# Performance work log

Measured on AMD Instinct MI355X. Metric: run time of the kernel, lower is better.

Reference implementation:

```python
import jax, jax.numpy as jnp
import numpy as np

N = 200000          # number of nodes (objects)
H = 64              # hidden_size
ARITIES = [1, 2, 3] # arity per relation
NTUP = [250000, 250000, 250000]  # ground atoms per relation


def setup_inputs() -> dict:
    key = jax.random.key(0)
    ks = jax.random.split(key, 32)
    inp = {"node_states": jax.random.normal(ks[0], (N, H), jnp.float32)}
    i = 1
    for r, (a, t) in enumerate(zip(ARITIES, NTUP)):
        inp[f"rel{r}_idx"] = jax.random.randint(ks[i], (t * a,), 0, N, dtype=jnp.int32).astype(jnp.int64); i += 1
        d = a * H
        s = (2.0 / d) ** 0.5
        inp[f"w1_r{r}"] = jax.random.normal(ks[i], (d, d), jnp.float32) * s; i += 1
        inp[f"b1_r{r}"] = jnp.zeros((d,), jnp.float32)
        inp[f"w2_r{r}"] = jax.random.normal(ks[i], (d, d), jnp.float32) * s; i += 1
        inp[f"b2_r{r}"] = jnp.zeros((d,), jnp.float32)
    su = (1.0 / (2 * H)) ** 0.5
    inp["wu1"] = jax.random.normal(ks[i], (2 * H, 2 * H), jnp.float32) * su; i += 1
    inp["bu1"] = jnp.zeros((2 * H,), jnp.float32)
    inp["wu2"] = jax.random.normal(ks[i], (2 * H, H), jnp.float32) * su
    inp["bu2"] = jnp.zeros((H,), jnp.float32)
    return inp


def reference(node_states, rel0_idx, rel1_idx, rel2_idx,
              w1_r0, b1_r0, w2_r0, b2_r0,
              w1_r1, b1_r1, w2_r1, b2_r1,
              w1_r2, b1_r2, w2_r2, b2_r2,
              wu1, bu1, wu2, bu2):
    sum_msg = jnp.zeros_like(node_states)
    rels = [(ARITIES[0], rel0_idx, w1_r0, b1_r0, w2_r0, b2_r0),
            (ARITIES[1], rel1_idx, w1_r1, b1_r1, w2_r1, b2_r1),
            (ARITIES[2], rel2_idx, w1_r2, b1_r2, w2_r2, b2_r2)]
    for a, idx, w1, b1, w2, b2 in rels:
        # gather node states for each ground atom: [T, a*H]
        x = node_states[idx].reshape(-1, a * H)
        h = jax.nn.relu(x @ w1 + b1)
        msg = (h @ w2 + b2).reshape(-1, H)  # [T*a, H]
        # scatter-add messages back to their nodes
        sum_msg = sum_msg.at[idx].add(msg)
    z = jnp.concatenate([sum_msg, node_states], axis=1)  # [N, 2H]
    return jax.nn.relu(z @ wu1 + bu1) @ wu2 + bu2
```

## Files before the change

### kernel.cpp

```cpp
#include <hip/hip_runtime.h>

#define H 64

typedef __attribute__((ext_vector_type(8))) __bf16 bf16x8;
typedef __attribute__((ext_vector_type(4))) float f32x4;
typedef unsigned short u16;
typedef unsigned int u32;

union F8 { bf16x8 b; u16 u[8]; uint4 q; };

__device__ __forceinline__ u16 f2bf(float f) {
    union { __bf16 h; u16 u; } v; v.h = (__bf16)f; return v.u;
}
__device__ __forceinline__ float bf2f(u16 x) {
    return __uint_as_float((u32)x << 16);
}
__device__ __forceinline__ unsigned swz(int col, int k, int K) {
    return ((unsigned)(col * K + k) * 2u) ^ (((unsigned)col & 7u) << 4);
}

struct Seg { const float* src; unsigned dstBytes; int K; int N; };
struct Segs { Seg s[8]; };

__global__ __launch_bounds__(256) void conv_weights(Segs segs, char* out) {
    Seg sg = segs.s[blockIdx.y];
    int total = sg.K * sg.N;
    char* dst = out + sg.dstBytes;
    for (int e = blockIdx.x * 256 + threadIdx.x; e < total; e += gridDim.x * 256) {
        int k = e / sg.N, n = e % sg.N;
        *(u16*)(dst + swz(n, k, sg.K)) = f2bf(sg.src[e]);
    }
}

__global__ __launch_bounds__(256) void conv_nodes(const float4* __restrict__ src,
                                                  ushort4* __restrict__ dst, int n4) {
    for (int i = blockIdx.x * 256 + threadIdx.x; i < n4; i += gridDim.x * 256) {
        float4 f = src[i];
        ushort4 o;
        o.x = f2bf(f.x); o.y = f2bf(f.y); o.z = f2bf(f.z); o.w = f2bf(f.w);
        dst[i] = o;
    }
}

__global__ __launch_bounds__(512) void scan_blocks(u32* __restrict__ data,
                                                   u32* __restrict__ sums, int n) {
    __shared__ u32 s[512];
    int tid = threadIdx.x, i = blockIdx.x * 512 + tid;
    u32 v = (i < n) ? data[i] : 0u;
    s[tid] = v; __syncthreads();
    for (int d = 1; d < 512; d <<= 1) {
        u32 t = (tid >= d) ? s[tid - d] : 0u; __syncthreads();
        s[tid] += t; __syncthreads();
    }
    if (i < n) data[i] = s[tid] - v;
    if (tid == 511) sums[blockIdx.x] = s[511];
}

__global__ __launch_bounds__(512) void scan_sums(u32* __restrict__ sums, int nb) {
    __shared__ u32 s[512];
    int tid = threadIdx.x;
    u32 v = (tid < nb) ? sums[tid] : 0u;
    s[tid] = v; __syncthreads();
    for (int d = 1; d < 512; d <<= 1) {
        u32 t = (tid >= d) ? s[tid - d] : 0u; __syncthreads();
        s[tid] += t; __syncthreads();
    }
    if (tid < nb) sums[tid] = s[tid] - v;
}

__global__ __launch_bounds__(512) void scan_add(u32* __restrict__ data,
                                                const u32* __restrict__ sums, int n) {
    int i = blockIdx.x * 512 + threadIdx.x;
    if (i < n) data[i] += sums[blockIdx.x];
}

struct OFix {
    const int* idx0; const int* idx1; const int* idx2;
    int m0, m1, m2;
    const u32* base; const u32* pre; u32* ord;
};

__global__ __launch_bounds__(256) void ord_fix(OFix a) {
    const int Mtot = a.m0 + a.m1 + a.m2;
    for (int e = blockIdx.x * 256 + threadIdx.x; e < Mtot; e += gridDim.x * 256) {
        int lm = e, node;
        if (lm < a.m0) node = a.idx0[lm];
        else { lm -= a.m0; if (lm < a.m1) node = a.idx1[lm]; else node = a.idx2[lm - a.m1]; }
        a.ord[a.base[node] + a.pre[e]] = (u32)e;
    }
}

template<int A>
__device__ __forceinline__ void msg_body(
    const u16* __restrict__ nsb, const int* __restrict__ idx,
    const u16* __restrict__ w1T, const float* __restrict__ b1,
    const u16* __restrict__ w2T, const float* __restrict__ b2,
    u16* __restrict__ msgR, int T, int bid, u16* Wl, u16* h1)
{
    constexpr int D    = A * 64;
    constexpr int KS   = D / 32;
    constexpr int NT   = D / 16;
    constexpr bool DUAL = (A == 1);
    constexpr bool CS   = (A > 1);
    constexpr int RF   = CS ? 2 : 1;
    constexpr int WH   = (A == 3) ? 3 : 1;
    constexpr int NTH  = NT / WH;
    constexpr int NTW  = CS ? NTH / 2 : NTH;
    constexpr int COLH = D / WH;
    constexpr int NPF  = (DUAL ? 2 * D * D : COLH * D) / 8 / 512;
    constexpr int NB   = WH * NTW;

    const int tid  = threadIdx.x;
    const int lane = tid & 63;
    const int w    = tid >> 6;
    const int g    = lane >> 4;
    const int lr   = lane & 15;
    const int rg   = CS ? (w >> 1) : w;
    const int cg   = CS ? (w & 1) : 0;

    const int tile = bid * 128;

    auto stage = [&](const u16* gsrc) {
#pragma unroll
        for (int i = 0; i < NPF; ++i) {
            const u16* gp = gsrc + ((i * 512 + tid) << 3);
            u16* lp = Wl + ((i * 512 + (w << 6)) << 3);
            __builtin_amdgcn_global_load_lds(
                (const __attribute__((address_space(1))) void*)gp,
                (__attribute__((address_space(3))) void*)lp, 16, 0, 0);
        }
    };

    bf16x8 a1[RF][KS];
#pragma unroll
    for (int rf = 0; rf < RF; ++rf) {
        const int trow = tile + rg * (16 * RF) + rf * 16 + lr;
        const int tl   = trow < T ? trow : T - 1;
        int nodes[A];
#pragma unroll
        for (int s = 0; s < A; ++s) nodes[s] = idx[(long)tl * A + s];
#pragma unroll
        for (int kk = 0; kk < KS; ++kk) {
            const u16* p = nsb + (long)nodes[kk >> 1] * H + ((kk & 1) * 32 + g * 8);
            F8 t; t.q = *(const uint4*)p;
            a1[rf][kk] = t.b;
        }
    }

    float bias1[NB], bias2[NB];
#pragma unroll
    for (int i = 0; i < NB; ++i) {
        const int jg = (i / NTW) * NTH + cg * NTW + (i % NTW);
        bias1[i] = b1[jg * 16 + lr];
        bias2[i] = b2[jg * 16 + lr];
    }

#pragma unroll
    for (int hh = 0; hh < WH; ++hh) {
        stage(DUAL ? w1T : (w1T + (size_t)hh * COLH * D));
        asm volatile("s_waitcnt vmcnt(0)" ::: "memory");
        __syncthreads();

#pragma unroll
        for (int jl = 0; jl < NTW; ++jl) {
            const int jc = cg * NTW + jl;
            const int jg = hh * NTH + jc;
            f32x4 acc0 = {0.f, 0.f, 0.f, 0.f};
            f32x4 acc1 = {0.f, 0.f, 0.f, 0.f};
#pragma unroll
            for (int kk = 0; kk < KS; ++kk) {
                F8 bf; bf.q = *(const uint4*)((const char*)Wl + swz(jc * 16 + lr, kk * 32 + g * 8, D));
                acc0 = __builtin_amdgcn_mfma_f32_16x16x32_bf16(a1[0][kk], bf.b, acc0, 0, 0, 0);
                if constexpr (CS)
                    acc1 = __builtin_amdgcn_mfma_f32_16x16x32_bf16(a1[1][kk], bf.b, acc1, 0, 0, 0);
            }
#pragma unroll
            for (int r = 0; r < 4; ++r) {
                const int row0 = rg * (16 * RF) + g * 4 + r;
                float v0 = acc0[r] + bias1[hh * NTW + jl]; v0 = v0 > 0.f ? v0 : 0.f;
                *(u16*)((char*)h1 + swz(row0, jg * 16 + lr, D)) = f2bf(v0);
                if constexpr (CS) {
                    float v1 = acc1[r] + bias1[hh * NTW + jl]; v1 = v1 > 0.f ? v1 : 0.f;
                    *(u16*)((char*)h1 + swz(row0 + 16, jg * 16 + lr, D)) = f2bf(v1);
                }
            }
        }
        if constexpr (!DUAL) __syncthreads();
    }

    bf16x8 a2[RF][KS];
#pragma unroll
    for (int rf = 0; rf < RF; ++rf) {
        const int row = rg * (16 * RF) + rf * 16 + lr;
#pragma unroll
        for (int kk = 0; kk < KS; ++kk) {
            F8 t; t.q = *(const uint4*)((const char*)h1 + swz(row, kk * 32 + g * 8, D));
            a2[rf][kk] = t.b;
        }
    }

#pragma unroll
    for (int hh = 0; hh < WH; ++hh) {
        if constexpr (!DUAL) {
            stage(w2T + (size_t)hh * COLH * D);
            asm volatile("s_waitcnt vmcnt(0)" ::: "memory");
            __syncthreads();
        }
        const char* W2base = DUAL ? (const char*)(Wl + D * D) : (const char*)Wl;

#pragma unroll
        for (int jl = 0; jl < NTW; ++jl) {
            const int jc = cg * NTW + jl;
            const int jg = hh * NTH + jc;
            f32x4 acc0 = {0.f, 0.f, 0.f, 0.f};
            f32x4 acc1 = {0.f, 0.f, 0.f, 0.f};
#pragma unroll
            for (int kk = 0; kk < KS; ++kk) {
                F8 bf; bf.q = *(const uint4*)(W2base + swz(jc * 16 + lr, kk * 32 + g * 8, D));
                acc0 = __builtin_amdgcn_mfma_f32_16x16x32_bf16(a2[0][kk], bf.b, acc0, 0, 0, 0);
                if constexpr (CS)
                    acc1 = __builtin_amdgcn_mfma_f32_16x16x32_bf16(a2[1][kk], bf.b, acc1, 0, 0, 0);
            }
            const int gc   = jg * 16 + lr;
            const int slot = gc >> 6;
            const int cs_  = gc & 63;
#pragma unroll
            for (int r = 0; r < 4; ++r) {
                const int a0 = rg * (16 * RF) + g * 4 + r;
                const int m0 = a0 * A + slot;
                unsigned b0 = (((unsigned)(m0 * 64 + cs_)) * 2u) ^ (((unsigned)m0 & 7u) << 4);
                *(u16*)((char*)h1 + b0) = f2bf(acc0[r] + bias2[hh * NTW + jl]);
                if constexpr (CS) {
                    const int m1 = (a0 + 16) * A + slot;
                    unsigned b1x = (((unsigned)(m1 * 64 + cs_)) * 2u) ^ (((unsigned)m1 & 7u) << 4);
                    *(u16*)((char*)h1 + b1x) = f2bf(acc1[r] + bias2[hh * NTW + jl]);
                }
            }
        }
        if constexpr (!DUAL) { if (hh + 1 < WH) __syncthreads(); }
    }

    if constexpr (CS) {
        __syncthreads();
        const int mbase = tile * A;
        constexpr int CH = 128 * A * 16;
#pragma unroll
        for (int i = 0; i < CH / 512; ++i) {
            const int c    = i * 512 + tid;
            const int row  = c >> 4;
            const int atom = row / A;
            if (tile + atom < T) {
                unsigned byte = (((unsigned)(row * 64 + (c & 15) * 4)) * 2u) ^ (((unsigned)row & 7u) << 4);
                uint2 v = *(const uint2*)((const char*)h1 + byte);
                *(uint2*)(msgR + (size_t)(mbase + row) * 64 + (c & 15) * 4) = v;
            }
        }
    } else {
        const int  mbase = (tile + w * 16) * A;
        const bool full  = (tile + 128 <= T);
#pragma unroll
        for (int i = 0; i < 16 * A; i += 4) {
            int ml   = i + (lane >> 4);
            int mrow = w * 16 * A + ml;
            bool ok  = full || ((tile + w * 16 + ml / A) < T);
            if (ok) {
                unsigned byte = (((unsigned)(mrow * 64 + (lane & 15) * 4)) * 2u) ^ (((unsigned)mrow & 7u) << 4);
                uint2 v = *(const uint2*)((const char*)h1 + byte);
                *(uint2*)(msgR + (size_t)((tile * A) + mrow) * 64 + (lane & 15) * 4) = v;
            }
        }
    }
}

struct MegaA {
    const u16* nsb;
    const int* idx0; const int* idx1; const int* idx2;
    int m0, m1, m2, t0, t1, t2;
    u32* cnt; u32* pre;
    const u16 *w10, *w20, *w11, *w21, *w12, *w22;
    const float *b10, *b20, *b11, *b21, *b12, *b22;
    u16* msgu;
    int nrank, nb2, nb1, nb0, striped;
};

__global__ __launch_bounds__(512, 4) void mega_kernel(MegaA a) {
    __shared__ __align__(16) u16 sm[36864];
    const int bx = blockIdx.x;
    int kind, id;
    if (a.striped) {
        const int strip = 4 * a.nrank;
        if (bx < strip) {
            if ((bx & 3) == 3) { kind = 1; id = bx >> 2; }
            else               { kind = 0; id = bx - (bx >> 2); }
        } else { kind = 0; id = bx - a.nrank; }
    } else {
        if (bx < a.nrank) { kind = 1; id = bx; }
        else              { kind = 0; id = bx - a.nrank; }
    }

    if (kind == 1) {
        const int Mtot = a.m0 + a.m1 + a.m2;
        for (int e = id * 512 + (int)threadIdx.x; e < Mtot; e += a.nrank * 512) {
            int lm = e, node;
            if (lm < a.m0) node = a.idx0[lm];
            else { lm -= a.m0; if (lm < a.m1) node = a.idx1[lm]; else node = a.idx2[lm - a.m1]; }
            a.pre[e] = atomicAdd(a.cnt + node, 1u);
        }
        return;
    }

    const int nmsg = a.nb2 + a.nb1 + a.nb0;
    if (id >= nmsg) return;
    if (id < a.nb2)
        msg_body<3>(a.nsb, a.idx2, a.w12, a.b12, a.w22, a.b22,
                    a.msgu + (size_t)(a.m0 + a.m1) * 64, a.t2, id, sm, sm + 12288);
    else if (id < a.nb2 + a.nb1)
        msg_body<2>(a.nsb, a.idx1, a.w11, a.b11, a.w21, a.b21,
                    a.msgu + (size_t)a.m0 * 64, a.t1, id - a.nb2, sm, sm + 16384);
    else
        msg_body<1>(a.nsb, a.idx0, a.w10, a.b10, a.w20, a.b20,
                    a.msgu, a.t0, id - a.nb2 - a.nb1, sm, sm + 8192);
}

template<int A>
__global__ __launch_bounds__(512) void rel_kernel(
    const float* __restrict__ ns, const int* __restrict__ idx,
    const u16* __restrict__ w1T, const float* __restrict__ b1,
    const u16* __restrict__ w2T, const float* __restrict__ b2,
    float* __restrict__ dout, int T)
{
    constexpr int D  = A * 64;
    constexpr int KS = D / 32;
    constexpr int NT = D / 16;
    constexpr bool DUAL = (A == 1);
    __shared__ __align__(16) u16 Wl[(DUAL ? 2 : 1) * D * D];
    __shared__ __align__(16) u16 h1[128 * D];

    const int tid  = threadIdx.x;
    const int lane = tid & 63;
    const int w    = tid >> 6;
    const int g    = lane >> 4;
    const int lr   = lane & 15;

    const int tile = blockIdx.x * 128;
    const int trow = tile + w * 16 + lr;
    const int tl   = trow < T ? trow : T - 1;

    {
        constexpr int NV = (DUAL ? 2 : 1) * D * D / 8;
        const uint4* s4 = (const uint4*)w1T;
        uint4* d4 = (uint4*)Wl;
#pragma unroll
        for (int i = 0; i < NV / 512; ++i) d4[i * 512 + tid] = s4[i * 512 + tid];
    }

    int nodes[A];
#pragma unroll
    for (int s = 0; s < A; ++s) nodes[s] = idx[(long)tl * A + s];

    bf16x8 a1[KS];
#pragma unroll
    for (int kk = 0; kk < KS; ++kk) {
        const float* p = ns + (long)nodes[kk >> 1] * H + ((kk & 1) * 32 + g * 8);
        float4 f0 = *(const float4*)p;
        float4 f1 = *(const float4*)(p + 4);
        F8 t;
        t.u[0] = f2bf(f0.x); t.u[1] = f2bf(f0.y); t.u[2] = f2bf(f0.z); t.u[3] = f2bf(f0.w);
        t.u[4] = f2bf(f1.x); t.u[5] = f2bf(f1.y); t.u[6] = f2bf(f1.z); t.u[7] = f2bf(f1.w);
        a1[kk] = t.b;
    }

    float bias1[NT];
#pragma unroll
    for (int j = 0; j < NT; ++j) bias1[j] = b1[j * 16 + lr];

    __syncthreads();

#pragma unroll
    for (int j = 0; j < NT; ++j) {
        f32x4 acc = {0.f, 0.f, 0.f, 0.f};
#pragma unroll
        for (int kk = 0; kk < KS; ++kk) {
            F8 bf; bf.q = *(const uint4*)((const char*)Wl + swz(j * 16 + lr, kk * 32 + g * 8, D));
            acc = __builtin_amdgcn_mfma_f32_16x16x32_bf16(a1[kk], bf.b, acc, 0, 0, 0);
        }
#pragma unroll
        for (int r = 0; r < 4; ++r) {
            float vv = acc[r] + bias1[j];
            vv = vv > 0.f ? vv : 0.f;
            int row = w * 16 + g * 4 + r;
            *(u16*)((char*)h1 + swz(row, j * 16 + lr, D)) = f2bf(vv);
        }
    }

    const char* W2base;
    if constexpr (!DUAL) {
        __syncthreads();
        const uint4* s4 = (const uint4*)w2T;
        uint4* d4 = (uint4*)Wl;
        constexpr int NV = D * D / 8;
#pragma unroll
        for (int i = 0; i < NV / 512; ++i) d4[i * 512 + tid] = s4[i * 512 + tid];
        W2base = (const char*)Wl;
    } else {
        W2base = (const char*)(Wl + D * D);
    }

    bf16x8 a2[KS];
#pragma unroll
    for (int kk = 0; kk < KS; ++kk) {
        int row = w * 16 + lr;
        F8 t; t.q = *(const uint4*)((const char*)h1 + swz(row, kk * 32 + g * 8, D));
        a2[kk] = t.b;
    }

    float bias2[NT];
#pragma unroll
    for (int j = 0; j < NT; ++j) bias2[j] = b2[j * 16 + lr];

    int  nodes2[A][4];
    bool pred[4];
#pragma unroll
    for (int r = 0; r < 4; ++r) {
        int t  = tile + w * 16 + g * 4 + r;
        int tc = t < T ? t : T - 1;
        pred[r] = t < T;
#pragma unroll
        for (int s = 0; s < A; ++s) nodes2[s][r] = idx[(long)tc * A + s];
    }
    if constexpr (!DUAL) __syncthreads();

#pragma unroll
    for (int j = 0; j < NT; ++j) {
        f32x4 acc = {0.f, 0.f, 0.f, 0.f};
#pragma unroll
        for (int kk = 0; kk < KS; ++kk) {
            F8 bf; bf.q = *(const uint4*)(W2base + swz(j * 16 + lr, kk * 32 + g * 8, D));
            acc = __builtin_amdgcn_mfma_f32_16x16x32_bf16(a2[kk], bf.b, acc, 0, 0, 0);
        }
        const int slot = j >> 2;
        const int coff = (j & 3) * 16 + lr;
#pragma unroll
        for (int r = 0; r < 4; ++r) {
            if (pred[r])
                unsafeAtomicAdd(dout + (long)nodes2[slot][r] * H + coff, acc[r] + bias2[j]);
        }
    }
}

template<bool SEG, bool NSB>
__global__ __launch_bounds__(512) void update_kernel(
    const float* __restrict__ ns, const u16* __restrict__ nsb,
    const float* __restrict__ sum,
    const u32* __restrict__ ord, const u32* __restrict__ base,
    const u16* __restrict__ msg, int Mtot,
    const u16* __restrict__ wu1T, const float* __restrict__ bu1,
    const u16* __restrict__ wu2T, const float* __restrict__ bu2,
    float* __restrict__ out, int N)
{
    __shared__ __align__(16) u16 Wl[128 * 128 + 64 * 128];
    __shared__ __align__(16) u16 h[128 * 128];

    const int tid  = threadIdx.x;
    const int lane = tid & 63;
    const int w    = tid >> 6;
    const int g    = lane >> 4;
    const int lr   = lane & 15;

    {
        const uint4* s4 = (const uint4*)wu1T;
        uint4* d4 = (uint4*)Wl;
#pragma unroll
        for (int i = 0; i < 6; ++i) d4[i * 512 + tid] = s4[i * 512 + tid];
    }

    const int tile = blockIdx.x * 128;
    const int trow = tile + w * 16 + lr;
    const int tl   = trow < N ? trow : N - 1;

    bf16x8 a1[4];
    if constexpr (SEG) {
        const u32 s = base[tl];
        const u32 e = (tl + 1 < N) ? base[tl + 1] : (u32)Mtot;
        float s0[8], s1[8];
#pragma unroll
        for (int j = 0; j < 8; ++j) { s0[j] = 0.f; s1[j] = 0.f; }
        for (u32 p = s; p < e; ++p) {
            const u16* row = msg + (size_t)ord[p] * 64;
            F8 v0, v1;
            v0.q = *(const uint4*)(row + g * 8);
            v1.q = *(const uint4*)(row + 32 + g * 8);
#pragma unroll
            for (int j = 0; j < 8; ++j) { s0[j] += bf2f(v0.u[j]); s1[j] += bf2f(v1.u[j]); }
        }
        F8 t0, t1;
#pragma unroll
        for (int j = 0; j < 8; ++j) { t0.u[j] = f2bf(s0[j]); t1.u[j] = f2bf(s1[j]); }
        a1[0] = t0.b; a1[1] = t1.b;
    } else {
#pragma unroll
        for (int kk = 0; kk < 2; ++kk) {
            int k = kk * 32 + g * 8;
            const float* p = sum + (long)tl * H + k;
            float4 f0 = *(const float4*)p;
            float4 f1 = *(const float4*)(p + 4);
            F8 t;
            t.u[0] = f2bf(f0.x); t.u[1] = f2bf(f0.y); t.u[2] = f2bf(f0.z); t.u[3] = f2bf(f0.w);
            t.u[4] = f2bf(f1.x); t.u[5] = f2bf(f1.y); t.u[6] = f2bf(f1.z); t.u[7] = f2bf(f1.w);
            a1[kk] = t.b;
        }
    }
#pragma unroll
    for (int kk = 2; kk < 4; ++kk) {
        if constexpr (NSB) {
            const u16* prow = nsb + (long)tl * H;
            F8 t; t.q = *(const uint4*)(prow + (kk - 2) * 32 + g * 8);
            a1[kk] = t.b;
        } else {
            int k = (kk - 2) * 32 + g * 8;
            const float* p = ns + (long)tl * H + k;
            float4 f0 = *(const float4*)p;
            float4 f1 = *(const float4*)(p + 4);
            F8 t;
            t.u[0] = f2bf(f0.x); t.u[1] = f2bf(f0.y); t.u[2] = f2bf(f0.z); t.u[3] = f2bf(f0.w);
            t.u[4] = f2bf(f1.x); t.u[5] = f2bf(f1.y); t.u[6] = f2bf(f1.z); t.u[7] = f2bf(f1.w);
            a1[kk] = t.b;
        }
    }

    float bias1[8], bias2[4];
#pragma unroll
    for (int j = 0; j < 8; ++j) bias1[j] = bu1[j * 16 + lr];
#pragma unroll
    for (int j = 0; j < 4; ++j) bias2[j] = bu2[j * 16 + lr];

    __syncthreads();

#pragma unroll
    for (int j = 0; j < 8; ++j) {
        f32x4 acc = {0.f, 0.f, 0.f, 0.f};
#pragma unroll
        for (int kk = 0; kk < 4; ++kk) {
            F8 bf; bf.q = *(const uint4*)((const char*)Wl + swz(j * 16 + lr, kk * 32 + g * 8, 128));
            acc = __builtin_amdgcn_mfma_f32_16x16x32_bf16(a1[kk], bf.b, acc, 0, 0, 0);
        }
#pragma unroll
        for (int r = 0; r < 4; ++r) {
            float vv = acc[r] + bias1[j];
            vv = vv > 0.f ? vv : 0.f;
            int row = w * 16 + g * 4 + r;
            *(u16*)((char*)h + swz(row, j * 16 + lr, 128)) = f2bf(vv);
        }
    }

    bf16x8 a2[4];
#pragma unroll
    for (int kk = 0; kk < 4; ++kk) {
        int row = w * 16 + lr;
        F8 t; t.q = *(const uint4*)((const char*)h + swz(row, kk * 32 + g * 8, 128));
        a2[kk] = t.b;
    }

    const char* W2base = (const char*)(Wl + 128 * 128);
#pragma unroll
    for (int j = 0; j < 4; ++j) {
        f32x4 acc = {0.f, 0.f, 0.f, 0.f};
#pragma unroll
        for (int kk = 0; kk < 4; ++kk) {
            F8 bf; bf.q = *(const uint4*)(W2base + swz(j * 16 + lr, kk * 32 + g * 8, 128));
            acc = __builtin_amdgcn_mfma_f32_16x16x32_bf16(a2[kk], bf.b, acc, 0, 0, 0);
        }
#pragma unroll
        for (int r = 0; r < 4; ++r) {
            int t = tile + w * 16 + g * 4 + r;
            if (t < N) out[(long)t * H + j * 16 + lr] = acc[r] + bias2[j];
        }
    }
}

extern "C" void kernel_launch(void* const* d_in, const int* in_sizes, int n_in,
                              void* d_out, int out_size, void* d_ws, size_t ws_size,
                              hipStream_t stream) {
    const float* ns = (const float*)d_in[0];
    const int* idxs[3] = { (const int*)d_in[1], (const int*)d_in[6], (const int*)d_in[11] };
    const float* b1s[3] = { (const float*)d_in[3], (const float*)d_in[8], (const float*)d_in[13] };
    const float* b2s[3] = { (const float*)d_in[5], (const float*)d_in[10], (const float*)d_in[15] };
    const float* bu1 = (const float*)d_in[17];
    const float* bu2 = (const float*)d_in[19];

    const int N = in_sizes[0] / H;
    const int Ts[3] = { in_sizes[1], in_sizes[6] / 2, in_sizes[11] / 3 };
    const int Ms[3] = { Ts[0] * 1, Ts[1] * 2, Ts[2] * 3 };
    const long Mtot = (long)Ms[0] + Ms[1] + Ms[2];

    char* wsb = (char*)d_ws;
    auto AL = [](size_t x) { return (x + 255) & ~(size_t)255; };

    const unsigned O_W1R0 = 0;
    const unsigned O_W2R0 = O_W1R0 + 64 * 64 * 2;
    const unsigned O_W1R1 = O_W2R0 + 64 * 64 * 2;
    const unsigned O_W2R1 = O_W1R1 + 128 * 128 * 2;
    const unsigned O_W1R2 = O_W2R1 + 128 * 128 * 2;
    const unsigned O_W2R2 = O_W1R2 + 192 * 192 * 2;
    const unsigned O_WU1  = O_W2R2 + 192 * 192 * 2;
    const unsigned O_WU2  = O_WU1 + 128 * 128 * 2;
    const size_t  wEnd    = O_WU2 + 128 * 64 * 2;
    const unsigned wOff1[3] = { O_W1R0, O_W1R1, O_W1R2 };
    const unsigned wOff2[3] = { O_W2R0, O_W2R1, O_W2R2 };

    const int nb = (N + 511) / 512;

    const size_t O_CNT = AL(wEnd);
    const size_t O_SUM = AL(O_CNT + (size_t)N * 4);
    const size_t O_PRE = AL(O_SUM + (size_t)nb * 4);
    const size_t O_ORD = AL(O_PRE + (size_t)Mtot * 4);
    const size_t O_NSB = AL(O_ORD + (size_t)Mtot * 4);
    const size_t nsLen = (size_t)N * H * 2;
    const size_t O_MSG = AL(O_NSB + nsLen);
    const size_t need  = O_MSG + (size_t)Mtot * 128;

    const bool sorted = (nb <= 512) && (ws_size >= need);

    Segs segs;
    segs.s[0] = {(const float*)d_in[2],  O_W1R0, 64, 64};
    segs.s[1] = {(const float*)d_in[4],  O_W2R0, 64, 64};
    segs.s[2] = {(const float*)d_in[7],  O_W1R1, 128, 128};
    segs.s[3] = {(const float*)d_in[9],  O_W2R1, 128, 128};
    segs.s[4] = {(const float*)d_in[12], O_W1R2, 192, 192};
    segs.s[5] = {(const float*)d_in[14], O_W2R2, 192, 192};
    segs.s[6] = {(const float*)d_in[16], O_WU1, 128, 128};
    segs.s[7] = {(const float*)d_in[18], O_WU2, 128, 64};

    float* dout = (float*)d_out;
    const u16* W1[3] = { (const u16*)(wsb + wOff1[0]), (const u16*)(wsb + wOff1[1]), (const u16*)(wsb + wOff1[2]) };
    const u16* W2[3] = { (const u16*)(wsb + wOff2[0]), (const u16*)(wsb + wOff2[1]), (const u16*)(wsb + wOff2[2]) };

    auto gT = [](int T) { return (T + 127) / 128; };

    if (sorted) {
        u32* cnt = (u32*)(wsb + O_CNT);
        u32* sums = (u32*)(wsb + O_SUM);
        u32* pre = (u32*)(wsb + O_PRE);
        u32* ord = (u32*)(wsb + O_ORD);
        u16* nsbp = (u16*)(wsb + O_NSB);
        u16* msgu = (u16*)(wsb + O_MSG);

        hipMemsetAsync(cnt, 0, (size_t)N * 4, stream);
        conv_weights<<<dim3(36, 8), 256, 0, stream>>>(segs, wsb);
        conv_nodes<<<1024, 256, 0, stream>>>((const float4*)ns, (ushort4*)nsbp, N * H / 4);

        const int nb0 = gT(Ts[0]), nb1 = gT(Ts[1]), nb2 = gT(Ts[2]);
        const int nmsg = nb0 + nb1 + nb2;
        int NR = nmsg / 3; if (NR > 1024) NR = 1024; if (NR < 1) NR = 1;
        const int striped = (nmsg >= 3 * NR) ? 1 : 0;
        const int NTOT = NR + nmsg;

        MegaA ma;
        ma.nsb = nsbp;
        ma.idx0 = idxs[0]; ma.idx1 = idxs[1]; ma.idx2 = idxs[2];
        ma.m0 = Ms[0]; ma.m1 = Ms[1]; ma.m2 = Ms[2];
        ma.t0 = Ts[0]; ma.t1 = Ts[1]; ma.t2 = Ts[2];
        ma.cnt = cnt; ma.pre = pre;
        ma.w10 = W1[0]; ma.w20 = W2[0];
        ma.w11 = W1[1]; ma.w21 = W2[1];
        ma.w12 = W1[2]; ma.w22 = W2[2];
        ma.b10 = b1s[0]; ma.b20 = b2s[0];
        ma.b11 = b1s[1]; ma.b21 = b2s[1];
        ma.b12 = b1s[2]; ma.b22 = b2s[2];
        ma.msgu = msgu;
        ma.nrank = NR; ma.nb2 = nb2; ma.nb1 = nb1; ma.nb0 = nb0; ma.striped = striped;
        mega_kernel<<<NTOT, 512, 0, stream>>>(ma);

        scan_blocks<<<nb, 512, 0, stream>>>(cnt, sums, N);
        scan_sums<<<1, 512, 0, stream>>>(sums, nb);
        scan_add<<<nb, 512, 0, stream>>>(cnt, sums, N);

        OFix fx;
        fx.idx0 = idxs[0]; fx.idx1 = idxs[1]; fx.idx2 = idxs[2];
        fx.m0 = Ms[0]; fx.m1 = Ms[1]; fx.m2 = Ms[2];
        fx.base = cnt; fx.pre = pre; fx.ord = ord;
        ord_fix<<<2048, 256, 0, stream>>>(fx);

        update_kernel<true, true><<<(N + 127) / 128, 512, 0, stream>>>(
            ns, nsbp, nullptr, ord, cnt, msgu, (int)Mtot,
            (const u16*)(wsb + O_WU1), bu1, (const u16*)(wsb + O_WU2), bu2, dout, N);
    } else {
        conv_weights<<<dim3(36, 8), 256, 0, stream>>>(segs, wsb);
        hipMemsetAsync(dout, 0, (size_t)N * H * sizeof(float), stream);
        for (int r = 0; r < 3; ++r) {
            const int T = Ts[r], nbl = gT(T);
            if (r == 0) rel_kernel<1><<<nbl, 512, 0, stream>>>(ns, idxs[0], W1[0], b1s[0], W2[0], b2s[0], dout, T);
            if (r == 1) rel_kernel<2><<<nbl, 512, 0, stream>>>(ns, idxs[1], W1[1], b1s[1], W2[1], b2s[1], dout, T);
            if (r == 2) rel_kernel<3><<<nbl, 512, 0, stream>>>(ns, idxs[2], W1[2], b1s[2], W2[2], b2s[2], dout, T);
        }
        update_kernel<false, false><<<(N + 127) / 128, 512, 0, stream>>>(
            ns, nullptr, dout, nullptr, nullptr, nullptr, 0,
            (const u16*)(wsb + O_WU1), bu1, (const u16*)(wsb + O_WU2), bu2, dout, N);
    }
}
```

Measured before the change: 271.3 us.

## Physically scatter messages into node-sorted order before segmented update reduction

Replaces the index permutation (ord) with a pass that copies each message row into its node-sorted slot. The update kernel then reduces contiguous rows instead of gathering through ord. This trades an extra full read and write of the message buffer for more coherent reads in the update kernel, and it needs a second message-sized workspace region. The ord path is kept as a fallback when workspace is insufficient.

```diff
diff --git a/kernel.cpp b/kernel.cpp
--- a/kernel.cpp
+++ b/kernel.cpp
@@ -87,6 +87,27 @@
         if (lm < a.m0) node = a.idx0[lm];
         else { lm -= a.m0; if (lm < a.m1) node = a.idx1[lm]; else node = a.idx2[lm - a.m1]; }
         a.ord[a.base[node] + a.pre[e]] = (u32)e;
+    }
+}
+
+struct Scat {
+    const int* idx0; const int* idx1; const int* idx2;
+    int m0, m1, m2;
+    const u32* base; const u32* pre;
+    const u16* msgu; u16* msgs;
+};
+
+__global__ __launch_bounds__(256) void scatter_msg(Scat a) {
+    const int Mtot = a.m0 + a.m1 + a.m2;
+    const int CH = Mtot * 8;
+    for (int c = blockIdx.x * 256 + threadIdx.x; c < CH; c += gridDim.x * 256) {
+        const int e = c >> 3, q = c & 7;
+        int lm = e, node;
+        if (lm < a.m0) node = a.idx0[lm];
+        else { lm -= a.m0; if (lm < a.m1) node = a.idx1[lm]; else node = a.idx2[lm - a.m1]; }
+        const u32 slot = a.base[node] + a.pre[e];
+        ((uint4*)(a.msgs + (size_t)slot * 64))[q] =
+            ((const uint4*)(a.msgu + (size_t)e * 64))[q];
     }
 }
 
@@ -256,7 +277,6 @@
             }
         }
     } else {
-        const int  mbase = (tile + w * 16) * A;
         const bool full  = (tile + 128 <= T);
 #pragma unroll
         for (int i = 0; i < 16 * A; i += 4) {
@@ -448,7 +468,7 @@
     }
 }
 
-template<bool SEG, bool NSB>
+template<int MODE>
 __global__ __launch_bounds__(512) void update_kernel(
     const float* __restrict__ ns, const u16* __restrict__ nsb,
     const float* __restrict__ sum,
@@ -479,14 +499,14 @@
     const int tl   = trow < N ? trow : N - 1;
 
     bf16x8 a1[4];
-    if constexpr (SEG) {
+    if constexpr (MODE <= 1) {
         const u32 s = base[tl];
         const u32 e = (tl + 1 < N) ? base[tl + 1] : (u32)Mtot;
         float s0[8], s1[8];
 #pragma unroll
         for (int j = 0; j < 8; ++j) { s0[j] = 0.f; s1[j] = 0.f; }
         for (u32 p = s; p < e; ++p) {
-            const u16* row = msg + (size_t)ord[p] * 64;
+            const u16* row = msg + (size_t)(MODE == 1 ? ord[p] : p) * 64;
             F8 v0, v1;
             v0.q = *(const uint4*)(row + g * 8);
             v1.q = *(const uint4*)(row + 32 + g * 8);
@@ -512,7 +532,7 @@
     }
 #pragma unroll
     for (int kk = 2; kk < 4; ++kk) {
-        if constexpr (NSB) {
+        if constexpr (MODE <= 1) {
             const u16* prow = nsb + (long)tl * H;
             F8 t; t.q = *(const uint4*)(prow + (kk - 2) * 32 + g * 8);
             a1[kk] = t.b;
@@ -617,9 +637,12 @@
     const size_t O_NSB = AL(O_ORD + (size_t)Mtot * 4);
     const size_t nsLen = (size_t)N * H * 2;
     const size_t O_MSG = AL(O_NSB + nsLen);
-    const size_t need  = O_MSG + (size_t)Mtot * 128;
-
-    const bool sorted = (nb <= 512) && (ws_size >= need);
+    const size_t O_MSGS = AL(O_MSG + (size_t)Mtot * 128);
+    const size_t need1 = O_MSGS;
+    const size_t need2 = O_MSGS + (size_t)Mtot * 128;
+
+    const bool sorted2 = (nb <= 512) && (ws_size >= need2);
+    const bool sorted1 = (nb <= 512) && (ws_size >= need1);
 
     Segs segs;
     segs.s[0] = {(const float*)d_in[2],  O_W1R0, 64, 64};
@@ -637,13 +660,14 @@
 
     auto gT = [](int T) { return (T + 127) / 128; };
 
-    if (sorted) {
+    if (sorted1 || sorted2) {
         u32* cnt = (u32*)(wsb + O_CNT);
         u32* sums = (u32*)(wsb + O_SUM);
         u32* pre = (u32*)(wsb + O_PRE);
         u32* ord = (u32*)(wsb + O_ORD);
         u16* nsbp = (u16*)(wsb + O_NSB);
         u16* msgu = (u16*)(wsb + O_MSG);
+        u16* msgs = (u16*)(wsb + O_MSGS);
 
         hipMemsetAsync(cnt, 0, (size_t)N * 4, stream);
         conv_weights<<<dim3(36, 8), 256, 0, stream>>>(segs, wsb);
@@ -675,15 +699,28 @@
         scan_sums<<<1, 512, 0, stream>>>(sums, nb);
         scan_add<<<nb, 512, 0, stream>>>(cnt, sums, N);
 
-        OFix fx;
-        fx.idx0 = idxs[0]; fx.idx1 = idxs[1]; fx.idx2 = idxs[2];
-        fx.m0 = Ms[0]; fx.m1 = Ms[1]; fx.m2 = Ms[2];
-        fx.base = cnt; fx.pre = pre; fx.ord = ord;
-        ord_fix<<<2048, 256, 0, stream>>>(fx);
-
-        update_kernel<true, true><<<(N + 127) / 128, 512, 0, stream>>>(
-            ns, nsbp, nullptr, ord, cnt, msgu, (int)Mtot,
-            (const u16*)(wsb + O_WU1), bu1, (const u16*)(wsb + O_WU2), bu2, dout, N);
+        if (sorted2) {
+            Scat sc;
+            sc.idx0 = idxs[0]; sc.idx1 = idxs[1]; sc.idx2 = idxs[2];
+            sc.m0 = Ms[0]; sc.m1 = Ms[1]; sc.m2 = Ms[2];
+            sc.base = cnt; sc.pre = pre;
+            sc.msgu = msgu; sc.msgs = msgs;
+            scatter_msg<<<2048, 256, 0, stream>>>(sc);
+
+            update_kernel<0><<<(N + 127) / 128, 512, 0, stream>>>(
+                ns, nsbp, nullptr, nullptr, cnt, msgs, (int)Mtot,
+                (const u16*)(wsb + O_WU1), bu1, (const u16*)(wsb + O_WU2), bu2, dout, N);
+        } else {
+            OFix fx;
+            fx.idx0 = idxs[0]; fx.idx1 = idxs[1]; fx.idx2 = idxs[2];
+            fx.m0 = Ms[0]; fx.m1 = Ms[1]; fx.m2 = Ms[2];
+            fx.base = cnt; fx.pre = pre; fx.ord = ord;
+            ord_fix<<<2048, 256, 0, stream>>>(fx);
+
+            update_kernel<1><<<(N + 127) / 128, 512, 0, stream>>>(
+                ns, nsbp, nullptr, ord, cnt, msgu, (int)Mtot,
+                (const u16*)(wsb + O_WU1), bu1, (const u16*)(wsb + O_WU2), bu2, dout, N);
+        }
     } else {
         conv_weights<<<dim3(36, 8), 256, 0, stream>>>(segs, wsb);
         hipMemsetAsync(dout, 0, (size_t)N * H * sizeof(float), stream);
@@ -693,7 +730,7 @@
             if (r == 1) rel_kernel<2><<<nbl, 512, 0, stream>>>(ns, idxs[1], W1[1], b1s[1], W2[1], b2s[1], dout, T);
             if (r == 2) rel_kernel<3><<<nbl, 512, 0, stream>>>(ns, idxs[2], W1[2], b1s[2], W2[2], b2s[2], dout, T);
         }
-        update_kernel<false, false><<<(N + 127) / 128, 512, 0, stream>>>(
+        update_kernel<2><<<(N + 127) / 128, 512, 0, stream>>>(
             ns, nullptr, dout, nullptr, nullptr, nullptr, 0,
             (const u16*)(wsb + O_WU1), bu1, (const u16*)(wsb + O_WU2), bu2, dout, N);
     }
```

After: 269.9 us. No clear change (-0.5%).
